# Kernel optimization log

Measured on AMD Instinct MI355X. Metric: run time of the kernel, lower is better.

The kernel has to match this reference:

```python
import jax, jax.numpy as jnp
import numpy as np

N_FULL = 50000
N_POOL = 12500
E_FULL = 600000
E_POOL = 150000
D = 128


def gcn_conv(x, W, b, edge_index, n):
    """GCNConv with self-loops and symmetric normalization.
    x: [n, d_in], W: [d_in, d_out], edge_index: [2, E] (src -> dst)."""
    xw = x @ W  # [n, d_out]
    loops = jnp.arange(n, dtype=edge_index.dtype)
    src = jnp.concatenate([edge_index[0], loops])
    dst = jnp.concatenate([edge_index[1], loops])
    deg = jnp.zeros((n,), dtype=xw.dtype).at[dst].add(1.0)  # >= 1 (self loops)
    dinv = jax.lax.rsqrt(deg)
    norm = (dinv[src] * dinv[dst])[:, None]  # [E+n, 1]
    out = jax.ops.segment_sum(xw[src] * norm, dst, num_segments=n)
    return out + b


def setup_inputs() -> dict:
    key = jax.random.key(0)
    ks = jax.random.split(key, 8)
    s = 1.0 / np.sqrt(D)
    return {
        "x": jnp.zeros((N_FULL, D), jnp.float32),
        "edge_index": jax.random.randint(ks[0], (2, E_FULL), 0, N_FULL, dtype=jnp.int64)
            if jax.config.jax_enable_x64 else jax.random.randint(ks[0], (2, E_FULL), 0, N_FULL).astype(jnp.int32),
        "pooled_x": jax.random.normal(ks[1], (N_POOL, D), jnp.float32),
        "pooled_edge_index": jax.random.randint(ks[2], (2, E_POOL), 0, N_POOL).astype(jnp.int32),
        "unpool_info": jnp.arange(N_POOL, dtype=jnp.int32),  # unique TopK-kept indices
        "W0": jax.random.normal(ks[3], (D, D), jnp.float32) * s,
        "b0": jnp.zeros((D,), jnp.float32),
        "W1": jax.random.normal(ks[4], (D, D), jnp.float32) * s,
        "b1": jnp.zeros((D,), jnp.float32),
        "W2": jax.random.normal(ks[5], (D, D), jnp.float32) * s,
        "b2": jnp.zeros((D,), jnp.float32),
    }


def reference(x, edge_index, pooled_x, pooled_edge_index, unpool_info,
              W0, b0, W1, b1, W2, b2):
    n = x.shape[0]
    # conv0 on the pooled graph + activation (ELU)
    h = jax.nn.elu(gcn_conv(pooled_x, W0, b0, pooled_edge_index, pooled_x.shape[0]))
    # TopKPool unpool: zero full graph, scatter pooled features to kept indices
    xf = jnp.zeros_like(x).at[unpool_info].set(h)
    # remaining convs on the full graph (dropout=0 / eval mode -> identity)
    xf = jax.nn.elu(gcn_conv(xf, W1, b1, edge_index, n))
    xf = jax.nn.elu(gcn_conv(xf, W2, b2, edge_index, n))
    return xf
```

## Files before the change

### kernel.cpp

```cpp
#include <hip/hip_runtime.h>
#include <math.h>

#define DD 128

static inline int cdiv(long a, long b){ return (int)((a + b - 1) / b); }

__device__ __forceinline__ unsigned bfpack(float a, float b){
  unsigned ua = __float_as_uint(a), ub = __float_as_uint(b);
  ua = (ua + 0x7fffu + ((ua >> 16) & 1u)) >> 16;
  ub = (ub + 0x7fffu + ((ub >> 16) & 1u)) >> 16;
  return ua | (ub << 16);
}

__global__ void k_count2(const int* __restrict__ dst_f, int Ef, int* __restrict__ cnt_f,
                         const int* __restrict__ dst_p, int Ep, int* __restrict__ cnt_p){
  int e = blockIdx.x * blockDim.x + threadIdx.x;
  if (e < Ef) atomicAdd(&cnt_f[dst_f[e]], 1);
  else { e -= Ef; if (e < Ep) atomicAdd(&cnt_p[dst_p[e]], 1); }
}

__global__ __launch_bounds__(256) void k_bsum(
    const int* __restrict__ cnt_f, int nf, const int* __restrict__ cnt_p, int np,
    int* __restrict__ bsum_f, int* __restrict__ bsum_p, int nbf, int nbp,
    const int* __restrict__ unpool, int* __restrict__ inv, int npool){
  int bi = blockIdx.x;
  if (bi >= nbf + nbp){
    int i = (bi - nbf - nbp) * 256 + threadIdx.x;
    if (i < npool) inv[unpool[i]] = i;
    return;
  }
  const int* cnt; int n; int* bsum; int b;
  if (bi < nbf){ cnt = cnt_f; n = nf; bsum = bsum_f; b = bi; }
  else         { cnt = cnt_p; n = np; bsum = bsum_p; b = bi - nbf; }
  __shared__ int s[256];
  int t = threadIdx.x;
  long base = (long)b * 1024 + t * 4;
  int v = 0;
  if (base + 3 < n){ int4 q = *(const int4*)(cnt + base); v = q.x + q.y + q.z + q.w; }
  else { for (int j = 0; j < 4; j++) if (base + j < n) v += cnt[base + j]; }
  s[t] = v; __syncthreads();
  for (int off = 128; off > 0; off >>= 1){ if (t < off) s[t] += s[t + off]; __syncthreads(); }
  if (t == 0) bsum[b] = s[0];
}

__global__ __launch_bounds__(128) void k_scan_b(int* __restrict__ bsum_f, int nbf,
                                                int* __restrict__ bsum_p, int nbp){
  __shared__ int s[128];
  int t = threadIdx.x;
  int v = (t < nbf) ? bsum_f[t] : 0;
  s[t] = v; __syncthreads();
  for (int off = 1; off < 128; off <<= 1){ int u = (t >= off) ? s[t - off] : 0; __syncthreads(); s[t] += u; __syncthreads(); }
  if (t < nbf) bsum_f[t] = s[t] - v;
  __syncthreads();
  int v2 = (t < nbp) ? bsum_p[t] : 0;
  s[t] = v2; __syncthreads();
  for (int off = 1; off < 128; off <<= 1){ int u = (t >= off) ? s[t - off] : 0; __syncthreads(); s[t] += u; __syncthreads(); }
  if (t < nbp) bsum_p[t] = s[t] - v2;
}

__global__ __launch_bounds__(256) void k_scan_f(
    const int* __restrict__ cnt_f, int nf, const int* __restrict__ bsum_f,
    const int* __restrict__ cnt_p, int np, const int* __restrict__ bsum_p,
    int* __restrict__ rptr_f, int* __restrict__ cur_f, float* __restrict__ dinv_f,
    int* __restrict__ rptr_p, int* __restrict__ cur_p, float* __restrict__ dinv_p,
    int nbf, int Ef, int Ep){
  const int* cnt; const int* bsum; int* rptr; int* cur; float* dinv; int n; int b;
  if ((int)blockIdx.x < nbf){ cnt=cnt_f; bsum=bsum_f; rptr=rptr_f; cur=cur_f; dinv=dinv_f; n=nf; b=blockIdx.x; }
  else                      { cnt=cnt_p; bsum=bsum_p; rptr=rptr_p; cur=cur_p; dinv=dinv_p; n=np; b=blockIdx.x-nbf; }
  __shared__ int s[256];
  int t = threadIdx.x;
  long base = (long)b * 1024 + t * 4;
  int c0=0,c1=0,c2=0,c3=0;
  if (base + 3 < n){ int4 q = *(const int4*)(cnt + base); c0=q.x; c1=q.y; c2=q.z; c3=q.w; }
  else {
    if (base + 0 < n) c0 = cnt[base + 0];
    if (base + 1 < n) c1 = cnt[base + 1];
    if (base + 2 < n) c2 = cnt[base + 2];
  }
  int tsum = c0 + c1 + c2 + c3;
  s[t] = tsum; __syncthreads();
  for (int off = 1; off < 256; off <<= 1){ int u = (t >= off) ? s[t - off] : 0; __syncthreads(); s[t] += u; __syncthreads(); }
  int run = bsum[b] + s[t] - tsum;
  int r0 = run, r1 = r0 + c0, r2 = r1 + c1, r3 = r2 + c2;
  if (base + 3 < n){
    *(int4*)(rptr + base) = make_int4(r0, r1, r2, r3);
    *(int4*)(cur + base)  = make_int4(r0, r1, r2, r3);
    dinv[base + 0] = rsqrtf((float)(c0 + 1));
    dinv[base + 1] = rsqrtf((float)(c1 + 1));
    dinv[base + 2] = rsqrtf((float)(c2 + 1));
    dinv[base + 3] = rsqrtf((float)(c3 + 1));
  } else {
    if (base + 0 < n){ rptr[base+0]=r0; cur[base+0]=r0; dinv[base+0]=rsqrtf((float)(c0+1)); }
    if (base + 1 < n){ rptr[base+1]=r1; cur[base+1]=r1; dinv[base+1]=rsqrtf((float)(c1+1)); }
    if (base + 2 < n){ rptr[base+2]=r2; cur[base+2]=r2; dinv[base+2]=rsqrtf((float)(c2+1)); }
  }
  if (blockIdx.x == 0 && t == 0){ rptr_f[nf] = Ef; rptr_p[np] = Ep; }
}

__global__ void k_fill2(const int* __restrict__ src_f, const int* __restrict__ dst_f, int Ef,
                        int* __restrict__ cur_f, int4* __restrict__ ewk_f,
                        const float* __restrict__ dinv_f, const int* __restrict__ inv,
                        const int* __restrict__ src_p, const int* __restrict__ dst_p, int Ep,
                        int* __restrict__ cur_p, int2* __restrict__ ewk_p,
                        const float* __restrict__ dinv_p){
  int e = blockIdx.x * blockDim.x + threadIdx.x;
  if (e < Ef){
    int s = src_f[e];
    int p = atomicAdd(&cur_f[dst_f[e]], 1);
    ewk_f[p] = make_int4(s, inv[s], __float_as_int(dinv_f[s]), 0);
  } else {
    e -= Ef;
    if (e < Ep){
      int s = src_p[e];
      int p = atomicAdd(&cur_p[dst_p[e]], 1);
      ewk_p[p] = make_int2(s, __float_as_int(dinv_p[s]));
    }
  }
}

__global__ __launch_bounds__(256) void k_gemm(const float* __restrict__ A,
                                              const float* __restrict__ W,
                                              float* __restrict__ C, int n){
  __shared__ float As[16][68];
  __shared__ float Ws[16][128];
  const int t    = threadIdx.x;
  const int row0 = blockIdx.x * 64;
  const int tc   = t & 15;
  const int tr   = t >> 4;
  const int sr   = t >> 2;
  const int sk   = (t & 3) * 4;

  float acc[4][8];
  #pragma unroll
  for (int i = 0; i < 4; i++)
    #pragma unroll
    for (int j = 0; j < 8; j++) acc[i][j] = 0.f;

  for (int kt = 0; kt < 128; kt += 16){
    float4 av = make_float4(0.f, 0.f, 0.f, 0.f);
    int arow = row0 + sr;
    if (arow < n) av = *(const float4*)(A + (long)arow * DD + kt + sk);
    const float4 wv0 = *(const float4*)(W + (long)(kt + tr) * DD + tc * 8);
    const float4 wv1 = *(const float4*)(W + (long)(kt + tr) * DD + tc * 8 + 4);
    __syncthreads();
    As[sk + 0][sr] = av.x;
    As[sk + 1][sr] = av.y;
    As[sk + 2][sr] = av.z;
    As[sk + 3][sr] = av.w;
    *(float4*)(&Ws[tr][tc * 8])     = wv0;
    *(float4*)(&Ws[tr][tc * 8 + 4]) = wv1;
    __syncthreads();
    #pragma unroll
    for (int k = 0; k < 16; k++){
      const float4 a4 = *(const float4*)(&As[k][tr * 4]);
      const float4 w0 = *(const float4*)(&Ws[k][tc * 8]);
      const float4 w1 = *(const float4*)(&Ws[k][tc * 8 + 4]);
      const float ar[4] = {a4.x, a4.y, a4.z, a4.w};
      const float wr[8] = {w0.x, w0.y, w0.z, w0.w, w1.x, w1.y, w1.z, w1.w};
      #pragma unroll
      for (int i = 0; i < 4; i++)
        #pragma unroll
        for (int j = 0; j < 8; j++)
          acc[i][j] += ar[i] * wr[j];
    }
  }
  #pragma unroll
  for (int i = 0; i < 4; i++){
    int row = row0 + tr * 4 + i;
    if (row < n){
      *(float4*)(C + (long)row * DD + tc * 8)     = make_float4(acc[i][0], acc[i][1], acc[i][2], acc[i][3]);
      *(float4*)(C + (long)row * DD + tc * 8 + 4) = make_float4(acc[i][4], acc[i][5], acc[i][6], acc[i][7]);
    }
  }
}

__global__ __launch_bounds__(256) void k_gemm_b(const float* __restrict__ A,
                                                const float* __restrict__ W,
                                                unsigned short* __restrict__ C, int n){
  __shared__ float As[16][68];
  __shared__ float Ws[16][128];
  const int t    = threadIdx.x;
  const int row0 = blockIdx.x * 64;
  const int tc   = t & 15;
  const int tr   = t >> 4;
  const int sr   = t >> 2;
  const int sk   = (t & 3) * 4;

  float acc[4][8];
  #pragma unroll
  for (int i = 0; i < 4; i++)
    #pragma unroll
    for (int j = 0; j < 8; j++) acc[i][j] = 0.f;

  for (int kt = 0; kt < 128; kt += 16){
    float4 av = make_float4(0.f, 0.f, 0.f, 0.f);
    int arow = row0 + sr;
    if (arow < n) av = *(const float4*)(A + (long)arow * DD + kt + sk);
    const float4 wv0 = *(const float4*)(W + (long)(kt + tr) * DD + tc * 8);
    const float4 wv1 = *(const float4*)(W + (long)(kt + tr) * DD + tc * 8 + 4);
    __syncthreads();
    As[sk + 0][sr] = av.x;
    As[sk + 1][sr] = av.y;
    As[sk + 2][sr] = av.z;
    As[sk + 3][sr] = av.w;
    *(float4*)(&Ws[tr][tc * 8])     = wv0;
    *(float4*)(&Ws[tr][tc * 8 + 4]) = wv1;
    __syncthreads();
    #pragma unroll
    for (int k = 0; k < 16; k++){
      const float4 a4 = *(const float4*)(&As[k][tr * 4]);
      const float4 w0 = *(const float4*)(&Ws[k][tc * 8]);
      const float4 w1 = *(const float4*)(&Ws[k][tc * 8 + 4]);
      const float ar[4] = {a4.x, a4.y, a4.z, a4.w};
      const float wr[8] = {w0.x, w0.y, w0.z, w0.w, w1.x, w1.y, w1.z, w1.w};
      #pragma unroll
      for (int i = 0; i < 4; i++)
        #pragma unroll
        for (int j = 0; j < 8; j++)
          acc[i][j] += ar[i] * wr[j];
    }
  }
  #pragma unroll
  for (int i = 0; i < 4; i++){
    int row = row0 + tr * 4 + i;
    if (row < n){
      uint4 pk;
      pk.x = bfpack(acc[i][0], acc[i][1]);
      pk.y = bfpack(acc[i][2], acc[i][3]);
      pk.z = bfpack(acc[i][4], acc[i][5]);
      pk.w = bfpack(acc[i][6], acc[i][7]);
      *(uint4*)(C + (long)row * DD + tc * 8) = pk;
    }
  }
}

__global__ __launch_bounds__(256) void k_agg_csr(const float* __restrict__ xw,
    const int* __restrict__ rptr, const int2* __restrict__ ewk,
    const float* __restrict__ dinv, const float* __restrict__ b,
    float* __restrict__ out, int n){
  int row = blockIdx.x * 4 + (threadIdx.x >> 6);
  if (row >= n) return;
  int c = (threadIdx.x & 63) * 2;
  int j0 = __builtin_amdgcn_readfirstlane(rptr[row]);
  int j1 = __builtin_amdgcn_readfirstlane(rptr[row + 1]);
  float ax[4], ay[4];
  #pragma unroll
  for (int i = 0; i < 4; i++){ ax[i] = 0.f; ay[i] = 0.f; }
  int j = j0;
  for (; j + 3 < j1; j += 4){
    #pragma unroll
    for (int i = 0; i < 4; i++){
      int2 q = ewk[j + i];
      float w = __int_as_float(q.y);
      float2 v = *(const float2*)(xw + (long)q.x * DD + c);
      ax[i] += v.x * w; ay[i] += v.y * w;
    }
  }
  for (; j < j1; j++){
    int2 q = ewk[j];
    float w = __int_as_float(q.y);
    float2 v = *(const float2*)(xw + (long)q.x * DD + c);
    ax[0] += v.x * w; ay[0] += v.y * w;
  }
  float sax = (ax[0]+ax[1]) + (ax[2]+ax[3]);
  float say = (ay[0]+ay[1]) + (ay[2]+ay[3]);
  float dd = dinv[row];
  float2 sv = *(const float2*)(xw + (long)row * DD + c);
  float2 bb = *(const float2*)(b + c);
  float vx = sax * dd + sv.x * dd * dd + bb.x;
  float vy = say * dd + sv.y * dd * dd + bb.y;
  vx = vx > 0.f ? vx : expm1f(vx);
  vy = vy > 0.f ? vy : expm1f(vy);
  *(float2*)(out + (long)row * DD + c) = make_float2(vx, vy);
}

__global__ __launch_bounds__(256) void k_agg_csr_b(const unsigned short* __restrict__ xwb,
    const int* __restrict__ rptr, const int4* __restrict__ ewk,
    const float* __restrict__ dinv, const float* __restrict__ b,
    float* __restrict__ out, int n){
  int row = blockIdx.x * 4 + (threadIdx.x >> 6);
  if (row >= n) return;
  int c = (threadIdx.x & 63) * 2;
  int j0 = __builtin_amdgcn_readfirstlane(rptr[row]);
  int j1 = __builtin_amdgcn_readfirstlane(rptr[row + 1]);
  float ax[8], ay[8];
  #pragma unroll
  for (int i = 0; i < 8; i++){ ax[i] = 0.f; ay[i] = 0.f; }
  int j = j0;
  for (; j + 7 < j1; j += 8){
    #pragma unroll
    for (int i = 0; i < 8; i++){
      int4 q = ewk[j + i];
      float w = __int_as_float(q.z);
      unsigned v = *(const unsigned*)(xwb + (long)q.x * DD + c);
      ax[i] += __uint_as_float(v << 16) * w;
      ay[i] += __uint_as_float(v & 0xffff0000u) * w;
    }
  }
  for (; j < j1; j++){
    int4 q = ewk[j];
    float w = __int_as_float(q.z);
    unsigned v = *(const unsigned*)(xwb + (long)q.x * DD + c);
    ax[0] += __uint_as_float(v << 16) * w;
    ay[0] += __uint_as_float(v & 0xffff0000u) * w;
  }
  float sax = ((ax[0]+ax[1])+(ax[2]+ax[3])) + ((ax[4]+ax[5])+(ax[6]+ax[7]));
  float say = ((ay[0]+ay[1])+(ay[2]+ay[3])) + ((ay[4]+ay[5])+(ay[6]+ay[7]));
  float dd = dinv[row];
  unsigned sv = *(const unsigned*)(xwb + (long)row * DD + c);
  float sx = __uint_as_float(sv << 16), sy = __uint_as_float(sv & 0xffff0000u);
  float2 bb = *(const float2*)(b + c);
  float vx = sax * dd + sx * dd * dd + bb.x;
  float vy = say * dd + sy * dd * dd + bb.y;
  vx = vx > 0.f ? vx : expm1f(vx);
  vy = vy > 0.f ? vy : expm1f(vy);
  *(float2*)(out + (long)row * DD + c) = make_float2(vx, vy);
}

__global__ __launch_bounds__(256) void k_agg_csr_sp(const float* __restrict__ hw,
    const int* __restrict__ inv, const int* __restrict__ rptr,
    const int4* __restrict__ ewk,
    const float* __restrict__ dinv, const float* __restrict__ b,
    float* __restrict__ out, int n){
  int row = blockIdx.x * 4 + (threadIdx.x >> 6);
  if (row >= n) return;
  int c = (threadIdx.x & 63) * 2;
  int j0 = __builtin_amdgcn_readfirstlane(rptr[row]);
  int j1 = __builtin_amdgcn_readfirstlane(rptr[row + 1]);
  float ax[4], ay[4];
  #pragma unroll
  for (int i = 0; i < 4; i++){ ax[i] = 0.f; ay[i] = 0.f; }
  int j = j0;
  for (; j + 3 < j1; j += 4){
    #pragma unroll
    for (int i = 0; i < 4; i++){
      int4 q = ewk[j + i];
      float w = __int_as_float(q.z);
      if (q.y >= 0){
        float2 v = *(const float2*)(hw + (long)q.y * DD + c);
        ax[i] += v.x * w; ay[i] += v.y * w;
      }
    }
  }
  for (; j < j1; j++){
    int4 q = ewk[j];
    float w = __int_as_float(q.z);
    if (q.y >= 0){
      float2 v = *(const float2*)(hw + (long)q.y * DD + c);
      ax[0] += v.x * w; ay[0] += v.y * w;
    }
  }
  float sax = (ax[0]+ax[1]) + (ax[2]+ax[3]);
  float say = (ay[0]+ay[1]) + (ay[2]+ay[3]);
  float dd = dinv[row];
  int pr = inv[row];
  float sx = 0.f, sy = 0.f;
  if (pr >= 0){
    float2 sv = *(const float2*)(hw + (long)pr * DD + c);
    sx = sv.x; sy = sv.y;
  }
  float2 bb = *(const float2*)(b + c);
  float vx = sax * dd + sx * dd * dd + bb.x;
  float vy = say * dd + sy * dd * dd + bb.y;
  vx = vx > 0.f ? vx : expm1f(vx);
  vy = vy > 0.f ? vy : expm1f(vy);
  *(float2*)(out + (long)row * DD + c) = make_float2(vx, vy);
}

extern "C" void kernel_launch(void* const* d_in, const int* in_sizes, int n_in,
                              void* d_out, int out_size, void* d_ws, size_t ws_size,
                              hipStream_t stream) {
  const int*   edge   = (const int*)d_in[1];
  const float* px     = (const float*)d_in[2];
  const int*   pedge  = (const int*)d_in[3];
  const int*   unpool = (const int*)d_in[4];
  const float* W0 = (const float*)d_in[5]; const float* b0 = (const float*)d_in[6];
  const float* W1 = (const float*)d_in[7]; const float* b1 = (const float*)d_in[8];
  const float* W2 = (const float*)d_in[9]; const float* b2 = (const float*)d_in[10];
  const int n_full = in_sizes[0] / DD;
  const int E_full = in_sizes[1] / 2;
  const int n_pool = in_sizes[2] / DD;
  const int E_pool = in_sizes[3] / 2;
  float* out = (float*)d_out;

  char* w = (char*)d_ws;
  size_t off = 0;
  auto alloc = [&](size_t bytes) -> void* {
    void* p = (void*)(w + off);
    off += (bytes + 255) / 256 * 256;
    return p;
  };
  float* dinv_p = (float*)alloc((size_t)n_pool * 4);
  float* dinv_f = (float*)alloc((size_t)n_full * 4);
  int* cnt_p  = (int*)alloc((size_t)n_pool * 4);
  int* cnt_f  = (int*)alloc((size_t)n_full * 4);
  size_t cnt_span = (size_t)((char*)(cnt_f + n_full) - (char*)cnt_p);
  int* rptr_p = (int*)alloc((size_t)(n_pool + 1) * 4);
  int* rptr_f = (int*)alloc((size_t)(n_full + 1) * 4);
  int2* ewk_p = (int2*)alloc((size_t)E_pool * 8);
  int4* ewk_f = (int4*)alloc((size_t)E_full * 16);
  int* invm   = (int*)alloc((size_t)n_full * 4);
  const int nbf = cdiv(n_full, 1024), nbp = cdiv(n_pool, 1024);
  int* bsum_f = (int*)alloc((size_t)nbf * 4);
  int* bsum_p = (int*)alloc((size_t)nbp * 4);
  const size_t big = (size_t)n_full * DD * 4;
  float* bufA = (float*)alloc(big);
  float* bufB = (float*)alloc(big);

  const int* src_f = edge;          const int* dst_f = edge + E_full;
  const int* src_p = pedge;         const int* dst_p = pedge + E_pool;

  hipMemsetAsync(cnt_p, 0, cnt_span, stream);
  hipMemsetAsync(invm, 0xFF, (size_t)n_full * 4, stream);
  k_count2<<<cdiv((long)E_full + E_pool,256),256,0,stream>>>(dst_f, E_full, cnt_f, dst_p, E_pool, cnt_p);
  const int nbi = cdiv(n_pool, 256);
  k_bsum<<<nbf + nbp + nbi,256,0,stream>>>(cnt_f, n_full, cnt_p, n_pool, bsum_f, bsum_p,
                                           nbf, nbp, unpool, invm, n_pool);
  k_scan_b<<<1,128,0,stream>>>(bsum_f, nbf, bsum_p, nbp);
  k_scan_f<<<nbf + nbp,256,0,stream>>>(cnt_f, n_full, bsum_f, cnt_p, n_pool, bsum_p,
                                       rptr_f, cnt_f, dinv_f, rptr_p, cnt_p, dinv_p,
                                       nbf, E_full, E_pool);
  k_fill2<<<cdiv((long)E_full + E_pool,256),256,0,stream>>>(
      src_f, dst_f, E_full, cnt_f, ewk_f, dinv_f, invm,
      src_p, dst_p, E_pool, cnt_p, ewk_p, dinv_p);

  float* xw0 = bufA;
  float* h0  = bufB;
  float* hw1 = bufA;
  float* y1  = bufB;
  unsigned short* xw2b = (unsigned short*)bufA;

  k_gemm<<<cdiv(n_pool,64),256,0,stream>>>(px, W0, xw0, n_pool);
  k_agg_csr<<<cdiv(n_pool,4),256,0,stream>>>(xw0, rptr_p, ewk_p, dinv_p, b0, h0, n_pool);

  k_gemm<<<cdiv(n_pool,64),256,0,stream>>>(h0, W1, hw1, n_pool);
  k_agg_csr_sp<<<cdiv(n_full,4),256,0,stream>>>(hw1, invm, rptr_f, ewk_f, dinv_f, b1, y1, n_full);

  k_gemm_b<<<cdiv(n_full,64),256,0,stream>>>(y1, W2, xw2b, n_full);
  k_agg_csr_b<<<cdiv(n_full,4),256,0,stream>>>(xw2b, rptr_f, ewk_f, dinv_f, b2, out, n_full);
}
```

Baseline: 317.3 us.

## Enlarge GEMM tile to 128 rows with 8x8 microtile; unroll sparse aggregation by 8

The two GEMM kernels are merged into one template and each block now covers 128 rows, with every thread computing an 8x8 output microtile instead of 4x8. This raises arithmetic intensity per shared-memory load. The cost is more accumulator registers, lower occupancy, and half as many blocks on the small pooled graph. The sparse-input aggregation kernel also gets an 8-way unrolled edge loop with eight independent accumulators, to put more gather loads in flight.

```diff
diff --git a/kernel.cpp b/kernel.cpp
--- a/kernel.cpp
+++ b/kernel.cpp
@@ -118,118 +118,80 @@
   }
 }
 
-__global__ __launch_bounds__(256) void k_gemm(const float* __restrict__ A,
-                                              const float* __restrict__ W,
-                                              float* __restrict__ C, int n){
-  __shared__ float As[16][68];
+template <bool BF16OUT>
+__global__ __launch_bounds__(256) void k_gemm_t(const float* __restrict__ A,
+                                                const float* __restrict__ W,
+                                                void* __restrict__ Cout, int n){
+  __shared__ float As[16][132];
   __shared__ float Ws[16][128];
   const int t    = threadIdx.x;
-  const int row0 = blockIdx.x * 64;
+  const int row0 = blockIdx.x * 128;
   const int tc   = t & 15;
   const int tr   = t >> 4;
   const int sr   = t >> 2;
-  const int sk   = (t & 3) * 4;
-
-  float acc[4][8];
+  const int sq   = (t & 3) * 4;
+  const int wr   = t >> 4;
+  const int wq   = (t & 15) * 4;
+
+  float acc[8][8];
   #pragma unroll
-  for (int i = 0; i < 4; i++)
+  for (int i = 0; i < 8; i++)
     #pragma unroll
     for (int j = 0; j < 8; j++) acc[i][j] = 0.f;
 
   for (int kt = 0; kt < 128; kt += 16){
-    float4 av = make_float4(0.f, 0.f, 0.f, 0.f);
-    int arow = row0 + sr;
-    if (arow < n) av = *(const float4*)(A + (long)arow * DD + kt + sk);
-    const float4 wv0 = *(const float4*)(W + (long)(kt + tr) * DD + tc * 8);
-    const float4 wv1 = *(const float4*)(W + (long)(kt + tr) * DD + tc * 8 + 4);
+    float4 a0 = make_float4(0.f,0.f,0.f,0.f), a1 = a0;
+    int r0 = row0 + sr, r1 = row0 + sr + 64;
+    if (r0 < n) a0 = *(const float4*)(A + (long)r0 * DD + kt + sq);
+    if (r1 < n) a1 = *(const float4*)(A + (long)r1 * DD + kt + sq);
+    const float4 wv0 = *(const float4*)(W + (long)(kt + wr) * DD + wq);
+    const float4 wv1 = *(const float4*)(W + (long)(kt + wr) * DD + wq + 64);
     __syncthreads();
-    As[sk + 0][sr] = av.x;
-    As[sk + 1][sr] = av.y;
-    As[sk + 2][sr] = av.z;
-    As[sk + 3][sr] = av.w;
-    *(float4*)(&Ws[tr][tc * 8])     = wv0;
-    *(float4*)(&Ws[tr][tc * 8 + 4]) = wv1;
+    As[sq + 0][sr]      = a0.x;  As[sq + 1][sr]      = a0.y;
+    As[sq + 2][sr]      = a0.z;  As[sq + 3][sr]      = a0.w;
+    As[sq + 0][sr + 64] = a1.x;  As[sq + 1][sr + 64] = a1.y;
+    As[sq + 2][sr + 64] = a1.z;  As[sq + 3][sr + 64] = a1.w;
+    *(float4*)(&Ws[wr][wq])      = wv0;
+    *(float4*)(&Ws[wr][wq + 64]) = wv1;
     __syncthreads();
     #pragma unroll
     for (int k = 0; k < 16; k++){
-      const float4 a4 = *(const float4*)(&As[k][tr * 4]);
-      const float4 w0 = *(const float4*)(&Ws[k][tc * 8]);
-      const float4 w1 = *(const float4*)(&Ws[k][tc * 8 + 4]);
-      const float ar[4] = {a4.x, a4.y, a4.z, a4.w};
-      const float wr[8] = {w0.x, w0.y, w0.z, w0.w, w1.x, w1.y, w1.z, w1.w};
+      const float4 af0 = *(const float4*)(&As[k][tr * 8]);
+      const float4 af1 = *(const float4*)(&As[k][tr * 8 + 4]);
+      const float4 wf0 = *(const float4*)(&Ws[k][tc * 8]);
+      const float4 wf1 = *(const float4*)(&Ws[k][tc * 8 + 4]);
+      const float ar[8] = {af0.x,af0.y,af0.z,af0.w,af1.x,af1.y,af1.z,af1.w};
+      const float wv[8] = {wf0.x,wf0.y,wf0.z,wf0.w,wf1.x,wf1.y,wf1.z,wf1.w};
       #pragma unroll
-      for (int i = 0; i < 4; i++)
+      for (int i = 0; i < 8; i++)
         #pragma unroll
         for (int j = 0; j < 8; j++)
-          acc[i][j] += ar[i] * wr[j];
-    }
-  }
-  #pragma unroll
-  for (int i = 0; i < 4; i++){
-    int row = row0 + tr * 4 + i;
-    if (row < n){
-      *(float4*)(C + (long)row * DD + tc * 8)     = make_float4(acc[i][0], acc[i][1], acc[i][2], acc[i][3]);
-      *(float4*)(C + (long)row * DD + tc * 8 + 4) = make_float4(acc[i][4], acc[i][5], acc[i][6], acc[i][7]);
-    }
-  }
-}
-
-__global__ __launch_bounds__(256) void k_gemm_b(const float* __restrict__ A,
-                                                const float* __restrict__ W,
-                                                unsigned short* __restrict__ C, int n){
-  __shared__ float As[16][68];
-  __shared__ float Ws[16][128];
-  const int t    = threadIdx.x;
-  const int row0 = blockIdx.x * 64;
-  const int tc   = t & 15;
-  const int tr   = t >> 4;
-  const int sr   = t >> 2;
-  const int sk   = (t & 3) * 4;
-
-  float acc[4][8];
-  #pragma unroll
-  for (int i = 0; i < 4; i++)
-    #pragma unroll
-    for (int j = 0; j < 8; j++) acc[i][j] = 0.f;
-
-  for (int kt = 0; kt < 128; kt += 16){
-    float4 av = make_float4(0.f, 0.f, 0.f, 0.f);
-    int arow = row0 + sr;
-    if (arow < n) av = *(const float4*)(A + (long)arow * DD + kt + sk);
-    const float4 wv0 = *(const float4*)(W + (long)(kt + tr) * DD + tc * 8);
-    const float4 wv1 = *(const float4*)(W + (long)(kt + tr) * DD + tc * 8 + 4);
-    __syncthreads();
-    As[sk + 0][sr] = av.x;
-    As[sk + 1][sr] = av.y;
-    As[sk + 2][sr] = av.z;
-    As[sk + 3][sr] = av.w;
-    *(float4*)(&Ws[tr][tc * 8])     = wv0;
-    *(float4*)(&Ws[tr][tc * 8 + 4]) = wv1;
-    __syncthreads();
-    #pragma unroll
-    for (int k = 0; k < 16; k++){
-      const float4 a4 = *(const float4*)(&As[k][tr * 4]);
-      const float4 w0 = *(const float4*)(&Ws[k][tc * 8]);
-      const float4 w1 = *(const float4*)(&Ws[k][tc * 8 + 4]);
-      const float ar[4] = {a4.x, a4.y, a4.z, a4.w};
-      const float wr[8] = {w0.x, w0.y, w0.z, w0.w, w1.x, w1.y, w1.z, w1.w};
-      #pragma unroll
-      for (int i = 0; i < 4; i++)
-        #pragma unroll
-        for (int j = 0; j < 8; j++)
-          acc[i][j] += ar[i] * wr[j];
-    }
-  }
-  #pragma unroll
-  for (int i = 0; i < 4; i++){
-    int row = row0 + tr * 4 + i;
-    if (row < n){
-      uint4 pk;
-      pk.x = bfpack(acc[i][0], acc[i][1]);
-      pk.y = bfpack(acc[i][2], acc[i][3]);
-      pk.z = bfpack(acc[i][4], acc[i][5]);
-      pk.w = bfpack(acc[i][6], acc[i][7]);
-      *(uint4*)(C + (long)row * DD + tc * 8) = pk;
+          acc[i][j] += ar[i] * wv[j];
+    }
+  }
+  if (BF16OUT){
+    unsigned short* C = (unsigned short*)Cout;
+    #pragma unroll
+    for (int i = 0; i < 8; i++){
+      int row = row0 + tr * 8 + i;
+      if (row < n){
+        uint4 pk;
+        pk.x = bfpack(acc[i][0], acc[i][1]);
+        pk.y = bfpack(acc[i][2], acc[i][3]);
+        pk.z = bfpack(acc[i][4], acc[i][5]);
+        pk.w = bfpack(acc[i][6], acc[i][7]);
+        *(uint4*)(C + (long)row * DD + tc * 8) = pk;
+      }
+    }
+  } else {
+    float* C = (float*)Cout;
+    #pragma unroll
+    for (int i = 0; i < 8; i++){
+      int row = row0 + tr * 8 + i;
+      if (row < n){
+        *(float4*)(C + (long)row * DD + tc * 8)     = make_float4(acc[i][0], acc[i][1], acc[i][2], acc[i][3]);
+        *(float4*)(C + (long)row * DD + tc * 8 + 4) = make_float4(acc[i][4], acc[i][5], acc[i][6], acc[i][7]);
+      }
     }
   }
 }
@@ -327,13 +289,13 @@
   int c = (threadIdx.x & 63) * 2;
   int j0 = __builtin_amdgcn_readfirstlane(rptr[row]);
   int j1 = __builtin_amdgcn_readfirstlane(rptr[row + 1]);
-  float ax[4], ay[4];
+  float ax[8], ay[8];
   #pragma unroll
-  for (int i = 0; i < 4; i++){ ax[i] = 0.f; ay[i] = 0.f; }
+  for (int i = 0; i < 8; i++){ ax[i] = 0.f; ay[i] = 0.f; }
   int j = j0;
-  for (; j + 3 < j1; j += 4){
-    #pragma unroll
-    for (int i = 0; i < 4; i++){
+  for (; j + 7 < j1; j += 8){
+    #pragma unroll
+    for (int i = 0; i < 8; i++){
       int4 q = ewk[j + i];
       float w = __int_as_float(q.z);
       if (q.y >= 0){
@@ -350,8 +312,8 @@
       ax[0] += v.x * w; ay[0] += v.y * w;
     }
   }
-  float sax = (ax[0]+ax[1]) + (ax[2]+ax[3]);
-  float say = (ay[0]+ay[1]) + (ay[2]+ay[3]);
+  float sax = ((ax[0]+ax[1])+(ax[2]+ax[3])) + ((ax[4]+ax[5])+(ax[6]+ax[7]));
+  float say = ((ay[0]+ay[1])+(ay[2]+ay[3])) + ((ay[4]+ay[5])+(ay[6]+ay[7]));
   float dd = dinv[row];
   int pr = inv[row];
   float sx = 0.f, sy = 0.f;
@@ -410,8 +372,8 @@
   const int* src_f = edge;          const int* dst_f = edge + E_full;
   const int* src_p = pedge;         const int* dst_p = pedge + E_pool;
 
-  hipMemsetAsync(cnt_p, 0, cnt_span, stream);
-  hipMemsetAsync(invm, 0xFF, (size_t)n_full * 4, stream);
+  (void)hipMemsetAsync(cnt_p, 0, cnt_span, stream);
+  (void)hipMemsetAsync(invm, 0xFF, (size_t)n_full * 4, stream);
   k_count2<<<cdiv((long)E_full + E_pool,256),256,0,stream>>>(dst_f, E_full, cnt_f, dst_p, E_pool, cnt_p);
   const int nbi = cdiv(n_pool, 256);
   k_bsum<<<nbf + nbp + nbi,256,0,stream>>>(cnt_f, n_full, cnt_p, n_pool, bsum_f, bsum_p,
@@ -430,12 +392,12 @@
   float* y1  = bufB;
   unsigned short* xw2b = (unsigned short*)bufA;
 
-  k_gemm<<<cdiv(n_pool,64),256,0,stream>>>(px, W0, xw0, n_pool);
+  k_gemm_t<false><<<cdiv(n_pool,128),256,0,stream>>>(px, W0, xw0, n_pool);
   k_agg_csr<<<cdiv(n_pool,4),256,0,stream>>>(xw0, rptr_p, ewk_p, dinv_p, b0, h0, n_pool);
 
-  k_gemm<<<cdiv(n_pool,64),256,0,stream>>>(h0, W1, hw1, n_pool);
+  k_gemm_t<false><<<cdiv(n_pool,128),256,0,stream>>>(h0, W1, hw1, n_pool);
   k_agg_csr_sp<<<cdiv(n_full,4),256,0,stream>>>(hw1, invm, rptr_f, ewk_f, dinv_f, b1, y1, n_full);
 
-  k_gemm_b<<<cdiv(n_full,64),256,0,stream>>>(y1, W2, xw2b, n_full);
+  k_gemm_t<true><<<cdiv(n_full,128),256,0,stream>>>(y1, W2, xw2b, n_full);
   k_agg_csr_b<<<cdiv(n_full,4),256,0,stream>>>(xw2b, rptr_f, ewk_f, dinv_f, b2, out, n_full);
 }
```

After: 324.2 us. +2.2%, slower.
